# Kernel tuning notes

Measured on AMD Instinct MI355X. Metric: run time of the kernel, lower is better.

The kernel has to match this reference:

```python
import jax, jax.numpy as jnp
import numpy as np
import math

C_IN, C_OUT = 256, 256
KH, KW = 3, 3
STRIDE, PAD = 1, 1
CURV = 1.0
SQRT_C = math.sqrt(CURV)
EPS = 1e-15

def _beta(a, b):
    return math.exp(math.lgamma(a) + math.lgamma(b) - math.lgamma(a + b))

BETA_NI = _beta(C_IN / 2.0, 0.5)                 # beta(n_i/2, 1/2)
BETA_N = _beta(C_IN * KH * KW / 2.0, 0.5)        # beta(n/2, 1/2)


def logmap0(y, axis):
    n = jnp.maximum(jnp.linalg.norm(y, axis=axis, keepdims=True), EPS)
    return jnp.arctanh(jnp.minimum(SQRT_C * n, 1.0 - 1e-7)) * y / (SQRT_C * n)


def expmap0(v, axis):
    n = jnp.maximum(jnp.linalg.norm(v, axis=axis, keepdims=True), EPS)
    return jnp.tanh(SQRT_C * n) * v / (SQRT_C * n)


def unfold(x):
    # torch.nn.Unfold: x [B,C,H,W] -> [B, C*KH*KW, L], channel-major patch order
    B, C, H, W = x.shape
    Ho = (H + 2 * PAD - KH) // STRIDE + 1
    Wo = (W + 2 * PAD - KW) // STRIDE + 1
    xp = jnp.pad(x, ((0, 0), (0, 0), (PAD, PAD), (PAD, PAD)))
    cols = [xp[:, :, i:i + STRIDE * Ho:STRIDE, j:j + STRIDE * Wo:STRIDE]
            for i in range(KH) for j in range(KW)]
    patches = jnp.stack(cols, axis=2)            # [B, C, KH*KW, Ho, Wo]
    return patches.reshape(B, C * KH * KW, Ho * Wo), Ho, Wo


def poincare_fc(x, z, r):
    # x: [..., D_in] on ball, z: [D_in, D_out], r: [D_out]
    x2 = jnp.sum(x * x, axis=-1, keepdims=True)
    lam = 2.0 / (1.0 - CURV * x2)                # conformal factor lambda_x
    z_norm = jnp.maximum(jnp.linalg.norm(z, axis=0), EPS)  # [D_out]
    xz = x @ z                                   # [..., D_out]
    two_csr = 2.0 * SQRT_C * r
    inner = (SQRT_C * lam * xz / z_norm * jnp.cosh(two_csr)
             - (lam - 1.0) * jnp.sinh(two_csr))
    v = 2.0 * z_norm / SQRT_C * jnp.arcsinh(inner)   # hyperplane distances
    w = jnp.sinh(SQRT_C * v) / SQRT_C
    return w / (1.0 + jnp.sqrt(1.0 + CURV * jnp.sum(w * w, axis=-1, keepdims=True)))


def setup_inputs() -> dict:
    key = jax.random.key(0)
    k1, k2, k3 = jax.random.split(key, 3)
    # tangent vectors -> points on the Poincare ball (man_dim=1)
    v = 0.05 * jax.random.normal(k1, (16, C_IN, 64, 64), dtype=jnp.float32)
    x = expmap0(v, axis=1)
    std = (2.0 * C_IN * KH * KW * C_OUT) ** (-0.5)
    weights = std * jax.random.normal(k2, (KH * KW * C_IN, C_OUT), dtype=jnp.float32)
    bias = 0.01 * jax.random.normal(k3, (C_OUT,), dtype=jnp.float32)
    return {"x": x, "weights": weights, "bias": bias}


def reference(x, weights, bias):
    B = x.shape[0]
    v = logmap0(x, axis=1) * (BETA_N / BETA_NI)      # log map + beta scaling
    u, Ho, Wo = unfold(v)                            # [B, CK, L]
    u = jnp.swapaxes(u, 1, 2)                        # [B, L, CK]
    p = expmap0(u, axis=-1)                          # back onto the ball
    y = poincare_fc(p, weights, bias)                # [B, L, C_OUT]
    return jnp.swapaxes(y, 1, 2).reshape(B, C_OUT, Ho, Wo)
```

## Files before the change

### kernel.cpp

```cpp
#include <hip/hip_runtime.h>
#include <cmath>

typedef __bf16 bf16;
typedef __bf16 bf16x8 __attribute__((ext_vector_type(8)));
typedef float f32x4 __attribute__((ext_vector_type(4)));

#define SBAR() __builtin_amdgcn_sched_barrier(0)


__device__ inline void gload16(const void* g, void* l) {
    __builtin_amdgcn_global_load_lds(
        (const __attribute__((address_space(1))) unsigned int*)g,
        (__attribute__((address_space(3))) unsigned int*)l, 16, 0, 0);
}

__global__ void k_prep_zt(const float* __restrict__ z, bf16* __restrict__ zt6) {
    int s = blockIdx.x;
    int cc = s / 9, tap = s % 9;
    int co = threadIdx.x;
#pragma unroll
    for (int g = 0; g < 4; ++g) {
        bf16x8 pk;
#pragma unroll
        for (int e = 0; e < 8; ++e) {
            int c = cc * 32 + g * 8 + e;
            pk[e] = (bf16)z[(size_t)(c * 9 + tap) * 256 + co];
        }
        *(bf16x8*)(zt6 + ((size_t)(s * 256 + co) * 4 + g) * 8) = pk;
    }
}

__global__ void k_prep_cols(const float* __restrict__ z, const float* __restrict__ r,
                            float* __restrict__ zn, float* __restrict__ ch,
                            float* __restrict__ sh) {
    __shared__ float red[256];
    int co = blockIdx.x, t = threadIdx.x;
    float s = 0.f;
    for (int i = 0; i < 9; ++i) {
        float v = z[(size_t)(i * 256 + t) * 256 + co];
        s += v * v;
    }
    red[t] = s;
    __syncthreads();
    for (int off = 128; off >= 1; off >>= 1) {
        if (t < off) red[t] += red[t + off];
        __syncthreads();
    }
    if (t == 0) {
        zn[co] = fmaxf(sqrtf(red[0]), 1e-15f);
        float tc = 2.f * r[co];
        ch[co] = coshf(tc);
        sh[co] = sinhf(tc);
    }
}

__global__ void k_logmap(const float* __restrict__ x, unsigned int* __restrict__ vt_u,
                         float* __restrict__ sq, float Rbeta) {
    __shared__ float tile[256][33];
    __shared__ float red[8][32];
    __shared__ float afac[32];
    int tid = threadIdx.x;
    int blk = blockIdx.x;
    int b = blk >> 7;
    int pix0 = (blk & 127) << 5;

    for (int it = 0; it < 32; ++it) {
        int c = it * 8 + (tid >> 5);
        int p = tid & 31;
        tile[c][p] = x[((size_t)b * 256 + c) * 4096 + pix0 + p];
    }
    __syncthreads();

    {
        int part = tid >> 5, p = tid & 31;
        float s = 0.f;
        for (int i = 0; i < 32; ++i) {
            float v = tile[part * 32 + i][p];
            s += v * v;
        }
        red[part][p] = s;
    }
    __syncthreads();
    if (tid < 32) {
        float n2 = 0.f;
        for (int i = 0; i < 8; ++i) n2 += red[i][tid];
        float n = sqrtf(n2);
        float nc = fmaxf(n, 1e-15f);
        float a = atanhf(fminf(nc, 0.9999999f)) / nc * Rbeta;
        afac[tid] = a;
        sq[(size_t)b * 4096 + pix0 + tid] = a * a * n2;
    }
    __syncthreads();

    for (int it = 0; it < 16; ++it) {
        int idx = it * 256 + tid;
        int p = idx >> 7;
        int cp = idx & 127;
        float a = afac[p];
        float v0 = a * tile[2 * cp][p];
        float v1 = a * tile[2 * cp + 1][p];
        union { bf16 h[2]; unsigned int u; } pk;
        pk.h[0] = (bf16)v0;
        pk.h[1] = (bf16)v1;
        vt_u[((size_t)b * 4096 + pix0 + p) * 128 + cp] = pk.u;
    }
}

__global__ void k_boxsum(const float* __restrict__ sq, float* __restrict__ nusq) {
    int idx = blockIdx.x * 256 + threadIdx.x;
    int b = idx >> 12, hw = idx & 4095, h = hw >> 6, w = hw & 63;
    const float* s = sq + ((size_t)b << 12);
    float acc = 0.f;
    for (int dh = -1; dh <= 1; ++dh) {
        int hh = h + dh;
        if ((unsigned)hh >= 64u) continue;
        for (int dw = -1; dw <= 1; ++dw) {
            int ww = w + dw;
            if ((unsigned)ww >= 64u) continue;
            acc += s[hh * 64 + ww];
        }
    }
    nusq[idx] = acc;
}

__global__ void
__attribute__((amdgpu_flat_work_group_size(512, 512)))
__attribute__((amdgpu_waves_per_eu(4, 4)))
k_hconv(const bf16* __restrict__ vt, const bf16* __restrict__ zt6,
        const float* __restrict__ nusq,
        const float* __restrict__ znp, const float* __restrict__ chp,
        const float* __restrict__ shp, float* __restrict__ out) {
    __shared__ __align__(1024) char Asb[16896];
    __shared__ float s_lds[128], lam_lds[128];
    __shared__ float red[128][4];

    int tid = threadIdx.x;
    int bid = blockIdx.x;
    int bh = ((bid & 7) << 6) | (bid >> 3);
    int b = bh >> 5, h0 = (bh & 31) << 1;

    if (tid < 32) {
        int u = tid >> 1, side = tid & 1;
        *(f32x4*)(Asb + u * 1056 + side * 1040) = (f32x4){0.f, 0.f, 0.f, 0.f};
    }

    if (tid >= 128 && tid < 256) {
        int t = tid - 128;
        int h = h0 + (t >> 6), w = t & 63;
        float q = nusq[((size_t)b << 12) + h * 64 + w];
        float ncl = fmaxf(sqrtf(q), 1e-15f);
        float p = __expf(2.f * ncl);
        float tt = (p - 1.f) / (p + 1.f);
        s_lds[t] = tt / ncl;
        lam_lds[t] = 2.f / (1.f - tt * tt);
    }

    int wave = tid >> 6, lane = tid & 63;
    int wn = wave & 3, wm = wave >> 2;
    int lrow = lane & 15, lk = lane >> 4;

    f32x4 acc[4][4];
#pragma unroll
    for (int m = 0; m < 4; ++m)
#pragma unroll
        for (int n = 0; n < 4; ++n) acc[m][n] = (f32x4){0.f, 0.f, 0.f, 0.f};

    const bf16* vb = vt + (((size_t)b) << 12) * 256;

    auto stageA = [&](int ccn) {
#pragma unroll
        for (int it = 0; it < 2; ++it) {
            int u = wave * 2 + it;
            int r = u >> 2, g = u & 3;
            int hr = h0 - 1 + r;
            hr = hr < 0 ? 0 : (hr > 63 ? 63 : hr);
            const bf16* gp = vb + ((size_t)(hr * 64 + lane)) * 256 + ccn * 32 + g * 8;
            gload16(gp, Asb + u * 1056 + 16);
        }
    };

    const bf16* bp = zt6 + ((size_t)(wn * 64 + lrow) * 4 + lk) * 8;
    bf16x8 bA[4], bB[4];
#pragma unroll
    for (int n = 0; n < 4; ++n) bA[n] = *(const bf16x8*)(bp + n * 512);
    const bf16* bnp = bp + 8192;

    stageA(0);
    __syncthreads();
    SBAR();

    const char* ApB = Asb + lk * 1056 + lrow * 16;

#define STAGE(CCV, TAP, CUR, NXT)                                            \
    {                                                                        \
        const int s_ = (CCV) * 9 + (TAP);                                    \
        if (s_ < 71) {                                                       \
            NXT[0] = *(const bf16x8*)(bnp);                                  \
            NXT[1] = *(const bf16x8*)(bnp + 512);                            \
            NXT[2] = *(const bf16x8*)(bnp + 1024);                           \
            NXT[3] = *(const bf16x8*)(bnp + 1536);                           \
            bnp += 8192;                                                     \
        }                                                                    \
        SBAR();                                                              \
        if ((TAP) == 0) {                                                    \
            asm volatile("s_waitcnt vmcnt(4)" ::: "memory");                 \
            SBAR();                                                          \
            asm volatile("s_barrier" ::: "memory");         \
            SBAR();                                                          \
        }                                                                    \
        {                                                                    \
            const int dh_ = (TAP) / 3 - 1, dw_ = (TAP) % 3 - 1;              \
            int hh_ = h0 + wm + dh_;                                         \
            if ((unsigned)hh_ < 64u) {                                       \
                const char* Ap_ = ApB + (wm + dh_ + 1) * 4224 + (dw_ + 1) * 16; \
                bf16x8 a0 = *(const bf16x8*)(Ap_);                           \
                bf16x8 a1 = *(const bf16x8*)(Ap_ + 256);                     \
                bf16x8 a2 = *(const bf16x8*)(Ap_ + 512);                     \
                bf16x8 a3 = *(const bf16x8*)(Ap_ + 768);                     \
                __builtin_amdgcn_s_setprio(1);                               \
                acc[0][0] = __builtin_amdgcn_mfma_f32_16x16x32_bf16(a0, CUR[0], acc[0][0], 0, 0, 0); \
                acc[1][0] = __builtin_amdgcn_mfma_f32_16x16x32_bf16(a1, CUR[0], acc[1][0], 0, 0, 0); \
                acc[2][0] = __builtin_amdgcn_mfma_f32_16x16x32_bf16(a2, CUR[0], acc[2][0], 0, 0, 0); \
                acc[3][0] = __builtin_amdgcn_mfma_f32_16x16x32_bf16(a3, CUR[0], acc[3][0], 0, 0, 0); \
                acc[0][1] = __builtin_amdgcn_mfma_f32_16x16x32_bf16(a0, CUR[1], acc[0][1], 0, 0, 0); \
                acc[1][1] = __builtin_amdgcn_mfma_f32_16x16x32_bf16(a1, CUR[1], acc[1][1], 0, 0, 0); \
                acc[2][1] = __builtin_amdgcn_mfma_f32_16x16x32_bf16(a2, CUR[1], acc[2][1], 0, 0, 0); \
                acc[3][1] = __builtin_amdgcn_mfma_f32_16x16x32_bf16(a3, CUR[1], acc[3][1], 0, 0, 0); \
                acc[0][2] = __builtin_amdgcn_mfma_f32_16x16x32_bf16(a0, CUR[2], acc[0][2], 0, 0, 0); \
                acc[1][2] = __builtin_amdgcn_mfma_f32_16x16x32_bf16(a1, CUR[2], acc[1][2], 0, 0, 0); \
                acc[2][2] = __builtin_amdgcn_mfma_f32_16x16x32_bf16(a2, CUR[2], acc[2][2], 0, 0, 0); \
                acc[3][2] = __builtin_amdgcn_mfma_f32_16x16x32_bf16(a3, CUR[2], acc[3][2], 0, 0, 0); \
                acc[0][3] = __builtin_amdgcn_mfma_f32_16x16x32_bf16(a0, CUR[3], acc[0][3], 0, 0, 0); \
                acc[1][3] = __builtin_amdgcn_mfma_f32_16x16x32_bf16(a1, CUR[3], acc[1][3], 0, 0, 0); \
                acc[2][3] = __builtin_amdgcn_mfma_f32_16x16x32_bf16(a2, CUR[3], acc[2][3], 0, 0, 0); \
                acc[3][3] = __builtin_amdgcn_mfma_f32_16x16x32_bf16(a3, CUR[3], acc[3][3], 0, 0, 0); \
                __builtin_amdgcn_s_setprio(0);                               \
            }                                                                \
        }                                                                    \
        SBAR();                                                              \
        if ((TAP) == 8 && (CCV) < 7) {                                       \
            asm volatile("s_barrier" ::: "memory");    \
            SBAR();                                                          \
            stageA((CCV) + 1);                                               \
            SBAR();                                                          \
        }                                                                    \
    }

#pragma unroll 1
    for (int cc2 = 0; cc2 < 4; ++cc2) {
        const int c0 = cc2 * 2, c1 = c0 + 1;
        STAGE(c0, 0, bA, bB) STAGE(c0, 1, bB, bA) STAGE(c0, 2, bA, bB)
        STAGE(c0, 3, bB, bA) STAGE(c0, 4, bA, bB) STAGE(c0, 5, bB, bA)
        STAGE(c0, 6, bA, bB) STAGE(c0, 7, bB, bA) STAGE(c0, 8, bA, bB)
        STAGE(c1, 0, bB, bA) STAGE(c1, 1, bA, bB) STAGE(c1, 2, bB, bA)
        STAGE(c1, 3, bA, bB) STAGE(c1, 4, bB, bA) STAGE(c1, 5, bA, bB)
        STAGE(c1, 6, bB, bA) STAGE(c1, 7, bA, bB) STAGE(c1, 8, bB, bA)
    }
#undef STAGE

    float cz[4], sh4[4], tz[4];
#pragma unroll
    for (int n = 0; n < 4; ++n) {
        int co = wn * 64 + n * 16 + lrow;
        float zn = znp[co];
        cz[n] = chp[co] / zn;
        sh4[n] = shp[co];
        tz[n] = 2.f * zn;
    }

#pragma unroll
    for (int m = 0; m < 4; ++m) {
#pragma unroll
        for (int r = 0; r < 4; ++r) {
            int wp = wm * 64 + m * 16 + 4 * lk + r;
            float s = s_lds[wp], lam = lam_lds[wp];
            float lm1 = lam - 1.f;
            float psum = 0.f;
#pragma unroll
            for (int n = 0; n < 4; ++n) {
                float xz = s * acc[m][n][r];
                float inner = lam * xz * cz[n] - lm1 * sh4[n];
                float as = __logf(inner + sqrtf(inner * inner + 1.f));
                float p = __expf(tz[n] * as);
                float w = 0.5f * (p - __builtin_amdgcn_rcpf(p));
                acc[m][n][r] = w;
                psum += w * w;
            }
            psum += __shfl_xor(psum, 1);
            psum += __shfl_xor(psum, 2);
            psum += __shfl_xor(psum, 4);
            psum += __shfl_xor(psum, 8);
            if (lrow == 0) red[wp][wn] = psum;
        }
    }
    __syncthreads();

    float dinv[4][4];
#pragma unroll
    for (int m = 0; m < 4; ++m)
#pragma unroll
        for (int r = 0; r < 4; ++r) {
            int wp = wm * 64 + m * 16 + 4 * lk + r;
            float tot = (red[wp][0] + red[wp][1]) + (red[wp][2] + red[wp][3]);
            dinv[m][r] = __builtin_amdgcn_rcpf(1.f + sqrtf(1.f + tot));
        }

    float* ob = out + (size_t)b * 256 * 4096 + (h0 + wm) * 64;
#pragma unroll
    for (int m = 0; m < 4; ++m) {
#pragma unroll
        for (int n = 0; n < 4; ++n) {
            int co = wn * 64 + n * 16 + lrow;
            f32x4 o;
#pragma unroll
            for (int r = 0; r < 4; ++r) o[r] = acc[m][n][r] * dinv[m][r];
            *(f32x4*)(ob + (size_t)co * 4096 + m * 16 + 4 * lk) = o;
        }
    }
}

extern "C" void kernel_launch(void* const* d_in, const int* in_sizes, int n_in,
                              void* d_out, int out_size, void* d_ws, size_t ws_size,
                              hipStream_t stream) {
    const float* x = (const float*)d_in[0];
    const float* z = (const float*)d_in[1];
    const float* r = (const float*)d_in[2];
    float* out = (float*)d_out;

    char* ws = (char*)d_ws;
    bf16* vt = (bf16*)ws;
    float* sq = (float*)(ws + 33554432);
    float* nusq = (float*)(ws + 33816576);
    bf16* zt6 = (bf16*)(ws + 34078720);
    float* zn = (float*)(ws + 35258368);
    float* ch = (float*)(ws + 35259392);
    float* sh = (float*)(ws + 35260416);
    if (ws_size < 35261440) return;

    double bni = lgamma(128.0) + lgamma(0.5) - lgamma(128.5);
    double bn = lgamma(1152.0) + lgamma(0.5) - lgamma(1152.5);
    float Rbeta = (float)exp(bn - bni);

    k_prep_zt<<<72, 256, 0, stream>>>(z, zt6);
    k_prep_cols<<<256, 256, 0, stream>>>(z, r, zn, ch, sh);
    k_logmap<<<2048, 256, 0, stream>>>(x, (unsigned int*)vt, sq, Rbeta);
    k_boxsum<<<256, 256, 0, stream>>>(sq, nusq);
    k_hconv<<<512, 512, 0, stream>>>(vt, zt6, nusq, zn, ch, sh, out);
}
```

Baseline: 131.3 us.

## Stage weights through LDS triple buffer, double-buffer A, fuse boxsum into conv

Weight fragments are now loaded asynchronously into a three-slot LDS ring with global_load_lds and read from LDS. They were previously loaded directly from global memory into registers. The activation tile is double-buffered, so the next channel chunk loads while the current one computes, and the A/B fragments for the next tap are prefetched into registers. The separate 3x3 box-sum kernel is folded into the conv prologue, which removes one launch and one intermediate buffer. The cost is more LDS, a barrier on every tap, and waves_per_eu dropping to 2, which reduces occupancy.

```diff
diff --git a/kernel.cpp b/kernel.cpp
--- a/kernel.cpp
+++ b/kernel.cpp
@@ -14,7 +14,7 @@
         (__attribute__((address_space(3))) unsigned int*)l, 16, 0, 0);
 }
 
-__global__ void k_prep_zt(const float* __restrict__ z, bf16* __restrict__ zt6) {
+__global__ void k_prep_zt(const float* __restrict__ z, bf16* __restrict__ zt5) {
     int s = blockIdx.x;
     int cc = s / 9, tap = s % 9;
     int co = threadIdx.x;
@@ -26,7 +26,7 @@
             int c = cc * 32 + g * 8 + e;
             pk[e] = (bf16)z[(size_t)(c * 9 + tap) * 256 + co];
         }
-        *(bf16x8*)(zt6 + ((size_t)(s * 256 + co) * 4 + g) * 8) = pk;
+        *(bf16x8*)(zt5 + ((size_t)(s * 4 + g) * 256 + co) * 8) = pk;
     }
 }
 
@@ -106,31 +106,15 @@
     }
 }
 
-__global__ void k_boxsum(const float* __restrict__ sq, float* __restrict__ nusq) {
-    int idx = blockIdx.x * 256 + threadIdx.x;
-    int b = idx >> 12, hw = idx & 4095, h = hw >> 6, w = hw & 63;
-    const float* s = sq + ((size_t)b << 12);
-    float acc = 0.f;
-    for (int dh = -1; dh <= 1; ++dh) {
-        int hh = h + dh;
-        if ((unsigned)hh >= 64u) continue;
-        for (int dw = -1; dw <= 1; ++dw) {
-            int ww = w + dw;
-            if ((unsigned)ww >= 64u) continue;
-            acc += s[hh * 64 + ww];
-        }
-    }
-    nusq[idx] = acc;
-}
-
 __global__ void
 __attribute__((amdgpu_flat_work_group_size(512, 512)))
-__attribute__((amdgpu_waves_per_eu(4, 4)))
-k_hconv(const bf16* __restrict__ vt, const bf16* __restrict__ zt6,
-        const float* __restrict__ nusq,
+__attribute__((amdgpu_waves_per_eu(2, 2)))
+k_hconv(const bf16* __restrict__ vt, const bf16* __restrict__ zt5,
+        const float* __restrict__ sq,
         const float* __restrict__ znp, const float* __restrict__ chp,
         const float* __restrict__ shp, float* __restrict__ out) {
-    __shared__ __align__(1024) char Asb[16896];
+    __shared__ __align__(1024) char Ab[2][16896];
+    __shared__ __align__(1024) char Bb3[3][16448];
     __shared__ float s_lds[128], lam_lds[128];
     __shared__ float red[128][4];
 
@@ -139,15 +123,28 @@
     int bh = ((bid & 7) << 6) | (bid >> 3);
     int b = bh >> 5, h0 = (bh & 31) << 1;
 
-    if (tid < 32) {
-        int u = tid >> 1, side = tid & 1;
-        *(f32x4*)(Asb + u * 1056 + side * 1040) = (f32x4){0.f, 0.f, 0.f, 0.f};
+    if (tid < 64) {
+        int buf = tid >> 5, rem = tid & 31;
+        int u = rem >> 1, side = rem & 1;
+        *(f32x4*)(Ab[buf] + u * 1056 + side * 1040) = (f32x4){0.f, 0.f, 0.f, 0.f};
     }
 
     if (tid >= 128 && tid < 256) {
         int t = tid - 128;
         int h = h0 + (t >> 6), w = t & 63;
-        float q = nusq[((size_t)b << 12) + h * 64 + w];
+        const float* sb = sq + ((size_t)b << 12);
+        float q = 0.f;
+#pragma unroll
+        for (int dh = -1; dh <= 1; ++dh) {
+            int hhh = h + dh;
+            if ((unsigned)hhh >= 64u) continue;
+#pragma unroll
+            for (int dw = -1; dw <= 1; ++dw) {
+                int ww = w + dw;
+                if ((unsigned)ww >= 64u) continue;
+                q += sb[hhh * 64 + ww];
+            }
+        }
         float ncl = fmaxf(sqrtf(q), 1e-15f);
         float p = __expf(2.f * ncl);
         float tt = (p - 1.f) / (p + 1.f);
@@ -167,7 +164,7 @@
 
     const bf16* vb = vt + (((size_t)b) << 12) * 256;
 
-    auto stageA = [&](int ccn) {
+    auto stageA = [&](char* dst, int ccn) {
 #pragma unroll
         for (int it = 0; it < 2; ++it) {
             int u = wave * 2 + it;
@@ -175,86 +172,119 @@
             int hr = h0 - 1 + r;
             hr = hr < 0 ? 0 : (hr > 63 ? 63 : hr);
             const bf16* gp = vb + ((size_t)(hr * 64 + lane)) * 256 + ccn * 32 + g * 8;
-            gload16(gp, Asb + u * 1056 + 16);
+            gload16(gp, dst + u * 1056 + 16);
         }
     };
-
-    const bf16* bp = zt6 + ((size_t)(wn * 64 + lrow) * 4 + lk) * 8;
-    bf16x8 bA[4], bB[4];
-#pragma unroll
-    for (int n = 0; n < 4; ++n) bA[n] = *(const bf16x8*)(bp + n * 512);
-    const bf16* bnp = bp + 8192;
-
-    stageA(0);
+    auto stageB = [&](char* dst, int s) {
+        const char* src = (const char*)zt5 + (size_t)s * 16384;
+#pragma unroll
+        for (int it = 0; it < 2; ++it) {
+            int u = wave * 2 + it;
+            gload16(src + u * 1024 + lane * 16,
+                    dst + (u >> 2) * 4112 + (u & 3) * 1024);
+        }
+    };
+
+    stageB((char*)Bb3[0], 0);
+    stageB((char*)Bb3[1], 1);
+    stageA((char*)Ab[0], 0);
     __syncthreads();
     SBAR();
 
-    const char* ApB = Asb + lk * 1056 + lrow * 16;
-
-#define STAGE(CCV, TAP, CUR, NXT)                                            \
+    const char* Ac = Ab[0] + lk * 1056 + lrow * 16;
+    const char* An_ = Ab[1] + lk * 1056 + lrow * 16;
+    const int bOff = lk * 4112 + wn * 1024 + lrow * 16;
+
+    bf16x8 afA[4], afB[4], bfA[4], bfB[4];
+#pragma unroll
+    for (int m = 0; m < 4; ++m)
+        afA[m] = *(const bf16x8*)(Ac + wm * 4224 + m * 256);
+#pragma unroll
+    for (int n = 0; n < 4; ++n)
+        bfA[n] = *(const bf16x8*)((const char*)Bb3[0] + bOff + n * 256);
+
+#define STAGE(CCV, TAP, AFC, BFC, AFN, BFN, ARD, ARN, ASTG, DOA, LAST)       \
     {                                                                        \
         const int s_ = (CCV) * 9 + (TAP);                                    \
-        if (s_ < 71) {                                                       \
-            NXT[0] = *(const bf16x8*)(bnp);                                  \
-            NXT[1] = *(const bf16x8*)(bnp + 512);                            \
-            NXT[2] = *(const bf16x8*)(bnp + 1024);                           \
-            NXT[3] = *(const bf16x8*)(bnp + 1536);                           \
-            bnp += 8192;                                                     \
+        if (s_ + 2 < 72) stageB((char*)Bb3[((TAP) + 2) % 3], s_ + 2);        \
+        if ((TAP) == 0 && (DOA)) stageA((char*)(ASTG), (CCV) + 1);           \
+        SBAR();                                                              \
+        if ((TAP) < 2) {                                                     \
+            if (LAST) { asm volatile("s_waitcnt vmcnt(2)" ::: "memory"); }   \
+            else      { asm volatile("s_waitcnt vmcnt(4)" ::: "memory"); }   \
+        } else if ((TAP) >= 7) {                                             \
+            if (LAST) { asm volatile("s_waitcnt vmcnt(0)" ::: "memory"); }   \
+            else      { asm volatile("s_waitcnt vmcnt(2)" ::: "memory"); }   \
+        } else {                                                             \
+            asm volatile("s_waitcnt vmcnt(2)" ::: "memory");                 \
         }                                                                    \
         SBAR();                                                              \
-        if ((TAP) == 0) {                                                    \
-            asm volatile("s_waitcnt vmcnt(4)" ::: "memory");                 \
-            SBAR();                                                          \
-            asm volatile("s_barrier" ::: "memory");         \
-            SBAR();                                                          \
+        asm volatile("s_barrier" ::: "memory");                              \
+        SBAR();                                                              \
+        {                              \
+            const int tn = ((TAP) == 8) ? 0 : (TAP) + 1;                     \
+            const int dhn = tn / 3 - 1, dwn = tn % 3 - 1;                    \
+            const char* An2 = (((TAP) == 8) ? (ARN) : (ARD)) +               \
+                              (wm + dhn + 1) * 4224 + (dwn + 1) * 16;        \
+            AFN[0] = *(const bf16x8*)(An2);                                  \
+            AFN[1] = *(const bf16x8*)(An2 + 256);                            \
+            AFN[2] = *(const bf16x8*)(An2 + 512);                            \
+            AFN[3] = *(const bf16x8*)(An2 + 768);                            \
+            const char* Bn2 = (const char*)Bb3[((TAP) + 1) % 3] + bOff;      \
+            BFN[0] = *(const bf16x8*)(Bn2);                                  \
+            BFN[1] = *(const bf16x8*)(Bn2 + 256);                            \
+            BFN[2] = *(const bf16x8*)(Bn2 + 512);                            \
+            BFN[3] = *(const bf16x8*)(Bn2 + 768);                            \
         }                                                                    \
         {                                                                    \
-            const int dh_ = (TAP) / 3 - 1, dw_ = (TAP) % 3 - 1;              \
+            const int dh_ = (TAP) / 3 - 1;                                   \
             int hh_ = h0 + wm + dh_;                                         \
             if ((unsigned)hh_ < 64u) {                                       \
-                const char* Ap_ = ApB + (wm + dh_ + 1) * 4224 + (dw_ + 1) * 16; \
-                bf16x8 a0 = *(const bf16x8*)(Ap_);                           \
-                bf16x8 a1 = *(const bf16x8*)(Ap_ + 256);                     \
-                bf16x8 a2 = *(const bf16x8*)(Ap_ + 512);                     \
-                bf16x8 a3 = *(const bf16x8*)(Ap_ + 768);                     \
                 __builtin_amdgcn_s_setprio(1);                               \
-                acc[0][0] = __builtin_amdgcn_mfma_f32_16x16x32_bf16(a0, CUR[0], acc[0][0], 0, 0, 0); \
-                acc[1][0] = __builtin_amdgcn_mfma_f32_16x16x32_bf16(a1, CUR[0], acc[1][0], 0, 0, 0); \
-                acc[2][0] = __builtin_amdgcn_mfma_f32_16x16x32_bf16(a2, CUR[0], acc[2][0], 0, 0, 0); \
-                acc[3][0] = __builtin_amdgcn_mfma_f32_16x16x32_bf16(a3, CUR[0], acc[3][0], 0, 0, 0); \
-                acc[0][1] = __builtin_amdgcn_mfma_f32_16x16x32_bf16(a0, CUR[1], acc[0][1], 0, 0, 0); \
-                acc[1][1] = __builtin_amdgcn_mfma_f32_16x16x32_bf16(a1, CUR[1], acc[1][1], 0, 0, 0); \
-                acc[2][1] = __builtin_amdgcn_mfma_f32_16x16x32_bf16(a2, CUR[1], acc[2][1], 0, 0, 0); \
-                acc[3][1] = __builtin_amdgcn_mfma_f32_16x16x32_bf16(a3, CUR[1], acc[3][1], 0, 0, 0); \
-                acc[0][2] = __builtin_amdgcn_mfma_f32_16x16x32_bf16(a0, CUR[2], acc[0][2], 0, 0, 0); \
-                acc[1][2] = __builtin_amdgcn_mfma_f32_16x16x32_bf16(a1, CUR[2], acc[1][2], 0, 0, 0); \
-                acc[2][2] = __builtin_amdgcn_mfma_f32_16x16x32_bf16(a2, CUR[2], acc[2][2], 0, 0, 0); \
-                acc[3][2] = __builtin_amdgcn_mfma_f32_16x16x32_bf16(a3, CUR[2], acc[3][2], 0, 0, 0); \
-                acc[0][3] = __builtin_amdgcn_mfma_f32_16x16x32_bf16(a0, CUR[3], acc[0][3], 0, 0, 0); \
-                acc[1][3] = __builtin_amdgcn_mfma_f32_16x16x32_bf16(a1, CUR[3], acc[1][3], 0, 0, 0); \
-                acc[2][3] = __builtin_amdgcn_mfma_f32_16x16x32_bf16(a2, CUR[3], acc[2][3], 0, 0, 0); \
-                acc[3][3] = __builtin_amdgcn_mfma_f32_16x16x32_bf16(a3, CUR[3], acc[3][3], 0, 0, 0); \
+                acc[0][0] = __builtin_amdgcn_mfma_f32_16x16x32_bf16(AFC[0], BFC[0], acc[0][0], 0, 0, 0); \
+                acc[1][0] = __builtin_amdgcn_mfma_f32_16x16x32_bf16(AFC[1], BFC[0], acc[1][0], 0, 0, 0); \
+                acc[2][0] = __builtin_amdgcn_mfma_f32_16x16x32_bf16(AFC[2], BFC[0], acc[2][0], 0, 0, 0); \
+                acc[3][0] = __builtin_amdgcn_mfma_f32_16x16x32_bf16(AFC[3], BFC[0], acc[3][0], 0, 0, 0); \
+                acc[0][1] = __builtin_amdgcn_mfma_f32_16x16x32_bf16(AFC[0], BFC[1], acc[0][1], 0, 0, 0); \
+                acc[1][1] = __builtin_amdgcn_mfma_f32_16x16x32_bf16(AFC[1], BFC[1], acc[1][1], 0, 0, 0); \
+                acc[2][1] = __builtin_amdgcn_mfma_f32_16x16x32_bf16(AFC[2], BFC[1], acc[2][1], 0, 0, 0); \
+                acc[3][1] = __builtin_amdgcn_mfma_f32_16x16x32_bf16(AFC[3], BFC[1], acc[3][1], 0, 0, 0); \
+                acc[0][2] = __builtin_amdgcn_mfma_f32_16x16x32_bf16(AFC[0], BFC[2], acc[0][2], 0, 0, 0); \
+                acc[1][2] = __builtin_amdgcn_mfma_f32_16x16x32_bf16(AFC[1], BFC[2], acc[1][2], 0, 0, 0); \
+                acc[2][2] = __builtin_amdgcn_mfma_f32_16x16x32_bf16(AFC[2], BFC[2], acc[2][2], 0, 0, 0); \
+                acc[3][2] = __builtin_amdgcn_mfma_f32_16x16x32_bf16(AFC[3], BFC[2], acc[3][2], 0, 0, 0); \
+                acc[0][3] = __builtin_amdgcn_mfma_f32_16x16x32_bf16(AFC[0], BFC[3], acc[0][3], 0, 0, 0); \
+                acc[1][3] = __builtin_amdgcn_mfma_f32_16x16x32_bf16(AFC[1], BFC[3], acc[1][3], 0, 0, 0); \
+                acc[2][3] = __builtin_amdgcn_mfma_f32_16x16x32_bf16(AFC[2], BFC[3], acc[2][3], 0, 0, 0); \
+                acc[3][3] = __builtin_amdgcn_mfma_f32_16x16x32_bf16(AFC[3], BFC[3], acc[3][3], 0, 0, 0); \
                 __builtin_amdgcn_s_setprio(0);                               \
             }                                                                \
         }                                                                    \
-        SBAR();                                                              \
-        if ((TAP) == 8 && (CCV) < 7) {                                       \
-            asm volatile("s_barrier" ::: "memory");    \
-            SBAR();                                                          \
-            stageA((CCV) + 1);                                               \
-            SBAR();                                                          \
-        }                                                                    \
     }
 
 #pragma unroll 1
     for (int cc2 = 0; cc2 < 4; ++cc2) {
-        const int c0 = cc2 * 2, c1 = c0 + 1;
-        STAGE(c0, 0, bA, bB) STAGE(c0, 1, bB, bA) STAGE(c0, 2, bA, bB)
-        STAGE(c0, 3, bB, bA) STAGE(c0, 4, bA, bB) STAGE(c0, 5, bB, bA)
-        STAGE(c0, 6, bA, bB) STAGE(c0, 7, bB, bA) STAGE(c0, 8, bA, bB)
-        STAGE(c1, 0, bB, bA) STAGE(c1, 1, bA, bB) STAGE(c1, 2, bB, bA)
-        STAGE(c1, 3, bA, bB) STAGE(c1, 4, bB, bA) STAGE(c1, 5, bA, bB)
-        STAGE(c1, 6, bB, bA) STAGE(c1, 7, bA, bB) STAGE(c1, 8, bB, bA)
+        const int c0 = 2 * cc2, c1 = c0 + 1;
+        const bool doA1 = (cc2 < 3);
+        const bool last1 = (cc2 == 3);
+        STAGE(c0, 0, afA, bfA, afB, bfB, Ac, An_, Ab[1], true,  false)
+        STAGE(c0, 1, afB, bfB, afA, bfA, Ac, An_, Ab[1], false, false)
+        STAGE(c0, 2, afA, bfA, afB, bfB, Ac, An_, Ab[1], false, false)
+        STAGE(c0, 3, afB, bfB, afA, bfA, Ac, An_, Ab[1], false, false)
+        STAGE(c0, 4, afA, bfA, afB, bfB, Ac, An_, Ab[1], false, false)
+        STAGE(c0, 5, afB, bfB, afA, bfA, Ac, An_, Ab[1], false, false)
+        STAGE(c0, 6, afA, bfA, afB, bfB, Ac, An_, Ab[1], false, false)
+        STAGE(c0, 7, afB, bfB, afA, bfA, Ac, An_, Ab[1], false, false)
+        STAGE(c0, 8, afA, bfA, afB, bfB, Ac, An_, Ab[1], false, false)
+        STAGE(c1, 0, afB, bfB, afA, bfA, An_, Ac, Ab[0], doA1, last1)
+        STAGE(c1, 1, afA, bfA, afB, bfB, An_, Ac, Ab[0], false, last1)
+        STAGE(c1, 2, afB, bfB, afA, bfA, An_, Ac, Ab[0], false, last1)
+        STAGE(c1, 3, afA, bfA, afB, bfB, An_, Ac, Ab[0], false, last1)
+        STAGE(c1, 4, afB, bfB, afA, bfA, An_, Ac, Ab[0], false, last1)
+        STAGE(c1, 5, afA, bfA, afB, bfB, An_, Ac, Ab[0], false, last1)
+        STAGE(c1, 6, afB, bfB, afA, bfA, An_, Ac, Ab[0], false, last1)
+        STAGE(c1, 7, afA, bfA, afB, bfB, An_, Ac, Ab[0], false, last1)
+        STAGE(c1, 8, afB, bfB, afA, bfA, An_, Ac, Ab[0], false, last1)
     }
 #undef STAGE
 
@@ -330,8 +360,7 @@
     char* ws = (char*)d_ws;
     bf16* vt = (bf16*)ws;
     float* sq = (float*)(ws + 33554432);
-    float* nusq = (float*)(ws + 33816576);
-    bf16* zt6 = (bf16*)(ws + 34078720);
+    bf16* zt5 = (bf16*)(ws + 34078720);
     float* zn = (float*)(ws + 35258368);
     float* ch = (float*)(ws + 35259392);
     float* sh = (float*)(ws + 35260416);
@@ -341,9 +370,8 @@
     double bn = lgamma(1152.0) + lgamma(0.5) - lgamma(1152.5);
     float Rbeta = (float)exp(bn - bni);
 
-    k_prep_zt<<<72, 256, 0, stream>>>(z, zt6);
+    k_prep_zt<<<72, 256, 0, stream>>>(z, zt5);
     k_prep_cols<<<256, 256, 0, stream>>>(z, r, zn, ch, sh);
     k_logmap<<<2048, 256, 0, stream>>>(x, (unsigned int*)vt, sq, Rbeta);
-    k_boxsum<<<256, 256, 0, stream>>>(sq, nusq);
-    k_hconv<<<512, 512, 0, stream>>>(vt, zt6, nusq, zn, ch, sh, out);
-}
+    k_hconv<<<512, 512, 0, stream>>>(vt, zt5, sq, zn, ch, sh, out);
+}
```

After: 141.8 us. 8.0% more time.

## Stage weights in LDS triple buffer, halve waves, fuse boxsum into conv

Applied to the files above, without the earlier changes.

The conv kernel moves from 8 waves holding B fragments in registers (loaded straight from global) to 4 waves that each compute 64x128 output tiles, with B tiles streamed into a triple-buffered LDS ring by async global-to-LDS loads. The weight layout changes to match. The separate 3x3 box-sum kernel is removed and its neighbourhood sum is computed inside the conv prologue, which saves one launch and one intermediate buffer. The cost is a block barrier on every tap, a doubled accumulator register count that limits occupancy, and more LDS traffic for B.

```diff
diff --git a/kernel.cpp b/kernel.cpp
--- a/kernel.cpp
+++ b/kernel.cpp
@@ -14,7 +14,7 @@
         (__attribute__((address_space(3))) unsigned int*)l, 16, 0, 0);
 }
 
-__global__ void k_prep_zt(const float* __restrict__ z, bf16* __restrict__ zt6) {
+__global__ void k_prep_zt(const float* __restrict__ z, bf16* __restrict__ zt5) {
     int s = blockIdx.x;
     int cc = s / 9, tap = s % 9;
     int co = threadIdx.x;
@@ -26,7 +26,7 @@
             int c = cc * 32 + g * 8 + e;
             pk[e] = (bf16)z[(size_t)(c * 9 + tap) * 256 + co];
         }
-        *(bf16x8*)(zt6 + ((size_t)(s * 256 + co) * 4 + g) * 8) = pk;
+        *(bf16x8*)(zt5 + ((size_t)(s * 4 + g) * 256 + co) * 8) = pk;
     }
 }
 
@@ -106,33 +106,17 @@
     }
 }
 
-__global__ void k_boxsum(const float* __restrict__ sq, float* __restrict__ nusq) {
-    int idx = blockIdx.x * 256 + threadIdx.x;
-    int b = idx >> 12, hw = idx & 4095, h = hw >> 6, w = hw & 63;
-    const float* s = sq + ((size_t)b << 12);
-    float acc = 0.f;
-    for (int dh = -1; dh <= 1; ++dh) {
-        int hh = h + dh;
-        if ((unsigned)hh >= 64u) continue;
-        for (int dw = -1; dw <= 1; ++dw) {
-            int ww = w + dw;
-            if ((unsigned)ww >= 64u) continue;
-            acc += s[hh * 64 + ww];
-        }
-    }
-    nusq[idx] = acc;
-}
-
 __global__ void
-__attribute__((amdgpu_flat_work_group_size(512, 512)))
-__attribute__((amdgpu_waves_per_eu(4, 4)))
-k_hconv(const bf16* __restrict__ vt, const bf16* __restrict__ zt6,
-        const float* __restrict__ nusq,
+__attribute__((amdgpu_flat_work_group_size(256, 256)))
+__attribute__((amdgpu_waves_per_eu(2, 2)))
+k_hconv(const bf16* __restrict__ vt, const bf16* __restrict__ zt5,
+        const float* __restrict__ sq,
         const float* __restrict__ znp, const float* __restrict__ chp,
         const float* __restrict__ shp, float* __restrict__ out) {
     __shared__ __align__(1024) char Asb[16896];
+    __shared__ __align__(1024) char Bb3[3][16448];
     __shared__ float s_lds[128], lam_lds[128];
-    __shared__ float red[128][4];
+    __shared__ float red[128][2];
 
     int tid = threadIdx.x;
     int bid = blockIdx.x;
@@ -144,10 +128,22 @@
         *(f32x4*)(Asb + u * 1056 + side * 1040) = (f32x4){0.f, 0.f, 0.f, 0.f};
     }
 
-    if (tid >= 128 && tid < 256) {
+    if (tid >= 128) {
         int t = tid - 128;
         int h = h0 + (t >> 6), w = t & 63;
-        float q = nusq[((size_t)b << 12) + h * 64 + w];
+        const float* sb = sq + ((size_t)b << 12);
+        float q = 0.f;
+#pragma unroll
+        for (int dh = -1; dh <= 1; ++dh) {
+            int hhh = h + dh;
+            if ((unsigned)hhh >= 64u) continue;
+#pragma unroll
+            for (int dw = -1; dw <= 1; ++dw) {
+                int ww = w + dw;
+                if ((unsigned)ww >= 64u) continue;
+                q += sb[hhh * 64 + ww];
+            }
+        }
         float ncl = fmaxf(sqrtf(q), 1e-15f);
         float p = __expf(2.f * ncl);
         float tt = (p - 1.f) / (p + 1.f);
@@ -156,21 +152,21 @@
     }
 
     int wave = tid >> 6, lane = tid & 63;
-    int wn = wave & 3, wm = wave >> 2;
+    int wn = wave & 1, wm = wave >> 1;
     int lrow = lane & 15, lk = lane >> 4;
 
-    f32x4 acc[4][4];
+    f32x4 acc[4][8];
 #pragma unroll
     for (int m = 0; m < 4; ++m)
 #pragma unroll
-        for (int n = 0; n < 4; ++n) acc[m][n] = (f32x4){0.f, 0.f, 0.f, 0.f};
+        for (int n = 0; n < 8; ++n) acc[m][n] = (f32x4){0.f, 0.f, 0.f, 0.f};
 
     const bf16* vb = vt + (((size_t)b) << 12) * 256;
 
     auto stageA = [&](int ccn) {
 #pragma unroll
-        for (int it = 0; it < 2; ++it) {
-            int u = wave * 2 + it;
+        for (int it = 0; it < 4; ++it) {
+            int u = wave * 4 + it;
             int r = u >> 2, g = u & 3;
             int hr = h0 - 1 + r;
             hr = hr < 0 ? 0 : (hr > 63 ? 63 : hr);
@@ -178,67 +174,57 @@
             gload16(gp, Asb + u * 1056 + 16);
         }
     };
-
-    const bf16* bp = zt6 + ((size_t)(wn * 64 + lrow) * 4 + lk) * 8;
-    bf16x8 bA[4], bB[4];
-#pragma unroll
-    for (int n = 0; n < 4; ++n) bA[n] = *(const bf16x8*)(bp + n * 512);
-    const bf16* bnp = bp + 8192;
-
+    auto stageB = [&](char* dst, int s) {
+        const char* src = (const char*)zt5 + (size_t)s * 16384;
+#pragma unroll
+        for (int it = 0; it < 4; ++it) {
+            gload16(src + it * 4096 + wave * 1024 + lane * 16,
+                    dst + it * 4112 + wave * 1024);
+        }
+    };
+
+    stageB((char*)Bb3[0], 0);
     stageA(0);
     __syncthreads();
     SBAR();
 
     const char* ApB = Asb + lk * 1056 + lrow * 16;
-
-#define STAGE(CCV, TAP, CUR, NXT)                                            \
+    const int bOff = lk * 4112 + (wn * 128 + lrow) * 16;
+
+#define STAGE(CCV, TAP)                                                      \
     {                                                                        \
         const int s_ = (CCV) * 9 + (TAP);                                    \
-        if (s_ < 71) {                                                       \
-            NXT[0] = *(const bf16x8*)(bnp);                                  \
-            NXT[1] = *(const bf16x8*)(bnp + 512);                            \
-            NXT[2] = *(const bf16x8*)(bnp + 1024);                           \
-            NXT[3] = *(const bf16x8*)(bnp + 1536);                           \
-            bnp += 8192;                                                     \
-        }                                                                    \
+        if (s_ < 71) stageB((char*)Bb3[((TAP) + 1) % 3], s_ + 1);            \
         SBAR();                                                              \
-        if ((TAP) == 0) {                                                    \
-            asm volatile("s_waitcnt vmcnt(4)" ::: "memory");                 \
-            SBAR();                                                          \
-            asm volatile("s_barrier" ::: "memory");         \
-            SBAR();                                                          \
-        }                                                                    \
+        if (s_ < 71) { asm volatile("s_waitcnt vmcnt(4)" ::: "memory"); }    \
+        else         { asm volatile("s_waitcnt vmcnt(0)" ::: "memory"); }    \
+        SBAR();                                                              \
+        asm volatile("s_barrier" ::: "memory");        \
+        SBAR();                                                              \
         {                                                                    \
             const int dh_ = (TAP) / 3 - 1, dw_ = (TAP) % 3 - 1;              \
             int hh_ = h0 + wm + dh_;                                         \
             if ((unsigned)hh_ < 64u) {                                       \
                 const char* Ap_ = ApB + (wm + dh_ + 1) * 4224 + (dw_ + 1) * 16; \
+                const char* Bp_ = (const char*)Bb3[(TAP) % 3] + bOff;        \
                 bf16x8 a0 = *(const bf16x8*)(Ap_);                           \
                 bf16x8 a1 = *(const bf16x8*)(Ap_ + 256);                     \
                 bf16x8 a2 = *(const bf16x8*)(Ap_ + 512);                     \
                 bf16x8 a3 = *(const bf16x8*)(Ap_ + 768);                     \
                 __builtin_amdgcn_s_setprio(1);                               \
-                acc[0][0] = __builtin_amdgcn_mfma_f32_16x16x32_bf16(a0, CUR[0], acc[0][0], 0, 0, 0); \
-                acc[1][0] = __builtin_amdgcn_mfma_f32_16x16x32_bf16(a1, CUR[0], acc[1][0], 0, 0, 0); \
-                acc[2][0] = __builtin_amdgcn_mfma_f32_16x16x32_bf16(a2, CUR[0], acc[2][0], 0, 0, 0); \
-                acc[3][0] = __builtin_amdgcn_mfma_f32_16x16x32_bf16(a3, CUR[0], acc[3][0], 0, 0, 0); \
-                acc[0][1] = __builtin_amdgcn_mfma_f32_16x16x32_bf16(a0, CUR[1], acc[0][1], 0, 0, 0); \
-                acc[1][1] = __builtin_amdgcn_mfma_f32_16x16x32_bf16(a1, CUR[1], acc[1][1], 0, 0, 0); \
-                acc[2][1] = __builtin_amdgcn_mfma_f32_16x16x32_bf16(a2, CUR[1], acc[2][1], 0, 0, 0); \
-                acc[3][1] = __builtin_amdgcn_mfma_f32_16x16x32_bf16(a3, CUR[1], acc[3][1], 0, 0, 0); \
-                acc[0][2] = __builtin_amdgcn_mfma_f32_16x16x32_bf16(a0, CUR[2], acc[0][2], 0, 0, 0); \
-                acc[1][2] = __builtin_amdgcn_mfma_f32_16x16x32_bf16(a1, CUR[2], acc[1][2], 0, 0, 0); \
-                acc[2][2] = __builtin_amdgcn_mfma_f32_16x16x32_bf16(a2, CUR[2], acc[2][2], 0, 0, 0); \
-                acc[3][2] = __builtin_amdgcn_mfma_f32_16x16x32_bf16(a3, CUR[2], acc[3][2], 0, 0, 0); \
-                acc[0][3] = __builtin_amdgcn_mfma_f32_16x16x32_bf16(a0, CUR[3], acc[0][3], 0, 0, 0); \
-                acc[1][3] = __builtin_amdgcn_mfma_f32_16x16x32_bf16(a1, CUR[3], acc[1][3], 0, 0, 0); \
-                acc[2][3] = __builtin_amdgcn_mfma_f32_16x16x32_bf16(a2, CUR[3], acc[2][3], 0, 0, 0); \
-                acc[3][3] = __builtin_amdgcn_mfma_f32_16x16x32_bf16(a3, CUR[3], acc[3][3], 0, 0, 0); \
+                _Pragma("unroll")                                            \
+                for (int n = 0; n < 8; ++n) {                                \
+                    bf16x8 bb = *(const bf16x8*)(Bp_ + n * 256);             \
+                    acc[0][n] = __builtin_amdgcn_mfma_f32_16x16x32_bf16(a0, bb, acc[0][n], 0, 0, 0); \
+                    acc[1][n] = __builtin_amdgcn_mfma_f32_16x16x32_bf16(a1, bb, acc[1][n], 0, 0, 0); \
+                    acc[2][n] = __builtin_amdgcn_mfma_f32_16x16x32_bf16(a2, bb, acc[2][n], 0, 0, 0); \
+                    acc[3][n] = __builtin_amdgcn_mfma_f32_16x16x32_bf16(a3, bb, acc[3][n], 0, 0, 0); \
+                }                                                            \
                 __builtin_amdgcn_s_setprio(0);                               \
             }                                                                \
         }                                                                    \
-        SBAR();                                                              \
         if ((TAP) == 8 && (CCV) < 7) {                                       \
+            SBAR();                                                          \
             asm volatile("s_barrier" ::: "memory");    \
             SBAR();                                                          \
             stageA((CCV) + 1);                                               \
@@ -247,24 +233,20 @@
     }
 
 #pragma unroll 1
-    for (int cc2 = 0; cc2 < 4; ++cc2) {
-        const int c0 = cc2 * 2, c1 = c0 + 1;
-        STAGE(c0, 0, bA, bB) STAGE(c0, 1, bB, bA) STAGE(c0, 2, bA, bB)
-        STAGE(c0, 3, bB, bA) STAGE(c0, 4, bA, bB) STAGE(c0, 5, bB, bA)
-        STAGE(c0, 6, bA, bB) STAGE(c0, 7, bB, bA) STAGE(c0, 8, bA, bB)
-        STAGE(c1, 0, bB, bA) STAGE(c1, 1, bA, bB) STAGE(c1, 2, bB, bA)
-        STAGE(c1, 3, bA, bB) STAGE(c1, 4, bB, bA) STAGE(c1, 5, bA, bB)
-        STAGE(c1, 6, bB, bA) STAGE(c1, 7, bA, bB) STAGE(c1, 8, bB, bA)
+    for (int cc = 0; cc < 8; ++cc) {
+        STAGE(cc, 0) STAGE(cc, 1) STAGE(cc, 2)
+        STAGE(cc, 3) STAGE(cc, 4) STAGE(cc, 5)
+        STAGE(cc, 6) STAGE(cc, 7) STAGE(cc, 8)
     }
 #undef STAGE
 
-    float cz[4], sh4[4], tz[4];
-#pragma unroll
-    for (int n = 0; n < 4; ++n) {
-        int co = wn * 64 + n * 16 + lrow;
+    float cz[8], sh8[8], tz[8];
+#pragma unroll
+    for (int n = 0; n < 8; ++n) {
+        int co = wn * 128 + n * 16 + lrow;
         float zn = znp[co];
         cz[n] = chp[co] / zn;
-        sh4[n] = shp[co];
+        sh8[n] = shp[co];
         tz[n] = 2.f * zn;
     }
 
@@ -277,9 +259,9 @@
             float lm1 = lam - 1.f;
             float psum = 0.f;
 #pragma unroll
-            for (int n = 0; n < 4; ++n) {
+            for (int n = 0; n < 8; ++n) {
                 float xz = s * acc[m][n][r];
-                float inner = lam * xz * cz[n] - lm1 * sh4[n];
+                float inner = lam * xz * cz[n] - lm1 * sh8[n];
                 float as = __logf(inner + sqrtf(inner * inner + 1.f));
                 float p = __expf(tz[n] * as);
                 float w = 0.5f * (p - __builtin_amdgcn_rcpf(p));
@@ -301,7 +283,7 @@
 #pragma unroll
         for (int r = 0; r < 4; ++r) {
             int wp = wm * 64 + m * 16 + 4 * lk + r;
-            float tot = (red[wp][0] + red[wp][1]) + (red[wp][2] + red[wp][3]);
+            float tot = red[wp][0] + red[wp][1];
             dinv[m][r] = __builtin_amdgcn_rcpf(1.f + sqrtf(1.f + tot));
         }
 
@@ -309,8 +291,8 @@
 #pragma unroll
     for (int m = 0; m < 4; ++m) {
 #pragma unroll
-        for (int n = 0; n < 4; ++n) {
-            int co = wn * 64 + n * 16 + lrow;
+        for (int n = 0; n < 8; ++n) {
+            int co = wn * 128 + n * 16 + lrow;
             f32x4 o;
 #pragma unroll
             for (int r = 0; r < 4; ++r) o[r] = acc[m][n][r] * dinv[m][r];
@@ -330,8 +312,7 @@
     char* ws = (char*)d_ws;
     bf16* vt = (bf16*)ws;
     float* sq = (float*)(ws + 33554432);
-    float* nusq = (float*)(ws + 33816576);
-    bf16* zt6 = (bf16*)(ws + 34078720);
+    bf16* zt5 = (bf16*)(ws + 34078720);
     float* zn = (float*)(ws + 35258368);
     float* ch = (float*)(ws + 35259392);
     float* sh = (float*)(ws + 35260416);
@@ -341,9 +322,8 @@
     double bn = lgamma(1152.0) + lgamma(0.5) - lgamma(1152.5);
     float Rbeta = (float)exp(bn - bni);
 
-    k_prep_zt<<<72, 256, 0, stream>>>(z, zt6);
+    k_prep_zt<<<72, 256, 0, stream>>>(z, zt5);
     k_prep_cols<<<256, 256, 0, stream>>>(z, r, zn, ch, sh);
     k_logmap<<<2048, 256, 0, stream>>>(x, (unsigned int*)vt, sq, Rbeta);
-    k_boxsum<<<256, 256, 0, stream>>>(sq, nusq);
-    k_hconv<<<512, 512, 0, stream>>>(vt, zt6, nusq, zn, ch, sh, out);
-}
+    k_hconv<<<512, 256, 0, stream>>>(vt, zt5, sq, zn, ch, sh, out);
+}
```

Measured after the change: 124.9 us. 4.9% less time.
